# Kernel optimization log

Hardware: AMD Instinct MI355X
Metric: run time of the kernel (lower is better)

Reference implementation:

```python
import jax, jax.numpy as jnp
import numpy as np

N, D, K, E = 100000, 256, 16, 3200000
COLLAPSE_REG = 0.1


def setup_inputs() -> dict:
    key = jax.random.key(0)
    k1, k2, k3 = jax.random.split(key, 3)
    features = jax.random.normal(k1, (N, D), dtype=jnp.float32)
    edge_index = jax.random.randint(k2, (2, E), 0, N, dtype=jnp.int32)
    adj_vals = jnp.ones((E,), dtype=jnp.float32)
    # orthogonal-ish init for linear weight, zero bias (as in nn.init.orthogonal_/zeros_)
    W = jax.random.normal(k3, (K, D), dtype=jnp.float32) / np.sqrt(D).astype(np.float32)
    b = jnp.zeros((K,), dtype=jnp.float32)
    return {"features": features, "edge_index": edge_index, "adj_vals": adj_vals, "W": W, "b": b}


def reference(features, edge_index, adj_vals, W, b):
    n = features.shape[0]
    k = W.shape[0]
    # cluster assignment: softmax(linear(features)); dropout_rate=0 -> identity
    assignments = jax.nn.softmax(features @ W.T + b, axis=-1)  # [n, k]

    rows, cols = edge_index[0], edge_index[1]
    # node degrees from sparse adjacency (row sums)
    degrees = jax.ops.segment_sum(adj_vals, rows, num_segments=n)  # [n]
    m2 = jnp.sum(degrees)  # 2m (total edge weight * 2)

    # SpMM: (A @ S) via edge-wise gather + segment-sum scatter
    AS = jax.ops.segment_sum(adj_vals[:, None] * assignments[cols], rows, num_segments=n)  # [n, k]
    graph_pooled = assignments.T @ AS  # [k, k] = S^T A S

    # modularity null-model normalizer: (S^T d)(d^T S) / 2m
    left = assignments.T @ degrees  # [k]
    normalizer = jnp.outer(left, left) / m2
    spectral_loss = -jnp.trace(graph_pooled - normalizer) / m2

    cluster_sizes = jnp.sum(assignments, axis=0)  # [k]
    collapse_loss = COLLAPSE_REG * (
        jnp.linalg.norm(cluster_sizes) / n * jnp.sqrt(jnp.float32(k)) - 1.0
    )

    # pooled cluster representations: selu((S / sizes)^T X)  -> [k, d]
    assignments_pooling = assignments / cluster_sizes  # broadcast over clusters
    features_pooled = jax.nn.selu(assignments_pooling.T @ features)
    return features_pooled, assignments, spectral_loss, collapse_loss
```

## Files before the change

### kernel.cpp

```cpp
#include <hip/hip_runtime.h>

#define N_NODES 100000
#define DIM 256
#define KC 16
#define NE 3200000
#define CHUNK 64
#define NCHUNKS ((N_NODES + CHUNK - 1) / CHUNK)

using bf16x8 = __attribute__((ext_vector_type(8))) short;
using f32x4  = __attribute__((ext_vector_type(4))) float;

__device__ __forceinline__ float bflo(unsigned u) { return __uint_as_float(u << 16); }
__device__ __forceinline__ unsigned short f2bf(float f) {
    unsigned u = __float_as_uint(f);
    return (unsigned short)((u + 0x7fffu + ((u >> 16) & 1u)) >> 16);
}
__device__ __forceinline__ unsigned packbf(float a, float b) {
    return (unsigned)f2bf(a) | ((unsigned)f2bf(b) << 16);
}

template <bool WRITE_PACK>
__global__ __launch_bounds__(256) void k_assign_stx(const float4* __restrict__ X4,
                                                    const float4* __restrict__ W4,
                                                    const float* __restrict__ bias,
                                                    float* __restrict__ S,
                                                    unsigned* __restrict__ Sb,
                                                    float* __restrict__ cs_g,
                                                    float* __restrict__ stx) {
    __shared__ unsigned short Xbf[CHUNK * 264];
    __shared__ float ps[CHUNK * 20];
    __shared__ float csred[4][KC];

    const int lane = threadIdx.x & 63;
    const int wv   = threadIdx.x >> 6;
    const int col  = lane & 15;
    const int quad = lane >> 4;
    const int d    = threadIdx.x;

    bf16x8 wfrag[8];
    #pragma unroll
    for (int s = 0; s < 8; s++) {
        float4 wa = W4[col * 64 + s * 8 + quad * 2];
        float4 wb = W4[col * 64 + s * 8 + quad * 2 + 1];
        union { bf16x8 v; unsigned u[4]; } wf;
        wf.u[0] = packbf(wa.x, wa.y);
        wf.u[1] = packbf(wa.z, wa.w);
        wf.u[2] = packbf(wb.x, wb.y);
        wf.u[3] = packbf(wb.z, wb.w);
        wfrag[s] = wf.v;
    }
    const float bk = bias[col];

    float st[KC];
    #pragma unroll
    for (int k = 0; k < KC; k++) st[k] = 0.f;
    float csacc = 0.f;

    for (int ch = blockIdx.x; ch < NCHUNKS; ch += gridDim.x) {
        const int base = ch * CHUNK;
        __syncthreads();

        {
            const int c4 = threadIdx.x & 63;
            const int r0 = threadIdx.x >> 6;
            #pragma unroll 4
            for (int s = 0; s < 16; s++) {
                int r = r0 + 4 * s;
                int rg = base + r;
                if (rg >= N_NODES) rg = N_NODES - 1;
                float4 x = X4[(size_t)rg * 64 + c4];
                *((uint2*)&Xbf[r * 264 + c4 * 4]) =
                    make_uint2(packbf(x.x, x.y), packbf(x.z, x.w));
            }
        }
        __syncthreads();

        f32x4 acc = {0.f, 0.f, 0.f, 0.f};
        #pragma unroll
        for (int s = 0; s < 8; s++) {
            bf16x8 a = *(const bf16x8*)&Xbf[(wv * 16 + col) * 264 + s * 32 + quad * 8];
            acc = __builtin_amdgcn_mfma_f32_16x16x32_bf16(a, wfrag[s], acc, 0, 0, 0);
        }
        #pragma unroll
        for (int r = 0; r < 4; r++) {
            float lg = acc[r] + bk;
            float m = lg;
            #pragma unroll
            for (int off = 8; off >= 1; off >>= 1) m = fmaxf(m, __shfl_xor(m, off));
            float e = __expf(lg - m);
            float ssum = e;
            #pragma unroll
            for (int off = 8; off >= 1; off >>= 1) ssum += __shfl_xor(ssum, off);
            float pv = e / ssum;

            int nd = base + wv * 16 + quad * 4 + r;
            bool val = (nd < N_NODES);
            if (!val) pv = 0.f;
            if (val) S[(size_t)nd * KC + col] = pv;
            ps[(wv * 16 + quad * 4 + r) * 20 + col] = pv;
            csacc += pv;
            if (WRITE_PACK) {
                unsigned qb = __float2uint_rn(pv * 255.f);
                unsigned p01 = qb | (((unsigned)__shfl_xor((int)qb, 1)) << 8);
                unsigned p0123 = p01 | (((unsigned)__shfl_xor((int)p01, 2)) << 16);
                if (val && !(col & 3))
                    Sb[(size_t)nd * 4 + (col >> 2)] = p0123;
            }
        }
        __syncthreads();

        #pragma unroll 4
        for (int i = 0; i < CHUNK; i++) {
            float x = bflo((unsigned)Xbf[i * 264 + d]);
            const float4* pp = (const float4*)&ps[i * 20];
            float4 p0 = pp[0], p1 = pp[1], p2 = pp[2], p3 = pp[3];
            st[0]  += p0.x * x; st[1]  += p0.y * x; st[2]  += p0.z * x; st[3]  += p0.w * x;
            st[4]  += p1.x * x; st[5]  += p1.y * x; st[6]  += p1.z * x; st[7]  += p1.w * x;
            st[8]  += p2.x * x; st[9]  += p2.y * x; st[10] += p2.z * x; st[11] += p2.w * x;
            st[12] += p3.x * x; st[13] += p3.y * x; st[14] += p3.z * x; st[15] += p3.w * x;
        }
    }

    #pragma unroll
    for (int k = 0; k < KC; k++) atomicAdd(&stx[k * DIM + d], st[k]);

    csacc += __shfl_xor(csacc, 16);
    csacc += __shfl_xor(csacc, 32);
    if (lane < KC) csred[wv][col] = csacc;
    __syncthreads();
    if (threadIdx.x < KC) {
        int t = threadIdx.x;
        atomicAdd(&cs_g[t], csred[0][t] + csred[1][t] + csred[2][t] + csred[3][t]);
    }
}

__device__ __forceinline__ void edge_acc_u8(uint4 qr, uint4 qc, float a,
                                            float (&lf)[KC], float& m2l, float& trl) {
    union { uint4 v; unsigned w[4]; } R, C;
    R.v = qr; C.v = qc;
    float dd = 0.f;
    #pragma unroll
    for (int q = 0; q < 4; q++) {
        unsigned x = R.w[q], y = C.w[q];
        float s0 = (float)(x & 0xffu);
        float s1 = (float)((x >> 8) & 0xffu);
        float s2 = (float)((x >> 16) & 0xffu);
        float s3 = (float)(x >> 24);
        float c0 = (float)(y & 0xffu);
        float c1 = (float)((y >> 8) & 0xffu);
        float c2 = (float)((y >> 16) & 0xffu);
        float c3 = (float)(y >> 24);
        dd = fmaf(s0, c0, dd); dd = fmaf(s1, c1, dd);
        dd = fmaf(s2, c2, dd); dd = fmaf(s3, c3, dd);
        lf[4 * q + 0] = fmaf(a, s0, lf[4 * q + 0]);
        lf[4 * q + 1] = fmaf(a, s1, lf[4 * q + 1]);
        lf[4 * q + 2] = fmaf(a, s2, lf[4 * q + 2]);
        lf[4 * q + 3] = fmaf(a, s3, lf[4 * q + 3]);
    }
    m2l += a;
    trl = fmaf(a, dd, trl);
}

__global__ __launch_bounds__(256) void k_edges_u8(const int* __restrict__ rows,
                                                  const int* __restrict__ cols,
                                                  const float* __restrict__ adj,
                                                  const uint4* __restrict__ Sb4,
                                                  float* __restrict__ m2_g,
                                                  float* __restrict__ tr_g,
                                                  float* __restrict__ left_g) {
    float m2l = 0.f, trl = 0.f;
    float lf[KC];
    #pragma unroll
    for (int k = 0; k < KC; k++) lf[k] = 0.f;

    const int NU = NE / 2;
    const int stride = gridDim.x * blockDim.x;
    for (int u = blockIdx.x * blockDim.x + threadIdx.x; u < NU; u += stride) {
        int2   r2 = *(const int2*)(rows + 2 * (size_t)u);
        int2   c2 = *(const int2*)(cols + 2 * (size_t)u);
        float2 a2 = *(const float2*)(adj + 2 * (size_t)u);
        uint4 qr0 = Sb4[r2.x];
        uint4 qc0 = Sb4[c2.x];
        uint4 qr1 = Sb4[r2.y];
        uint4 qc1 = Sb4[c2.y];
        edge_acc_u8(qr0, qc0, a2.x, lf, m2l, trl);
        edge_acc_u8(qr1, qc1, a2.y, lf, m2l, trl);
    }

    trl *= (1.f / 65025.f);
    #pragma unroll
    for (int k = 0; k < KC; k++) lf[k] *= (1.f / 255.f);

    #pragma unroll
    for (int off = 32; off >= 1; off >>= 1) {
        m2l += __shfl_xor(m2l, off);
        trl += __shfl_xor(trl, off);
    }
    #pragma unroll
    for (int k = 0; k < KC; k++) {
        float v = lf[k];
        #pragma unroll
        for (int off = 32; off >= 1; off >>= 1) v += __shfl_xor(v, off);
        lf[k] = v;
    }
    __shared__ float red[4][18];
    int w = threadIdx.x >> 6;
    if ((threadIdx.x & 63) == 0) {
        red[w][0] = m2l; red[w][1] = trl;
        #pragma unroll
        for (int k = 0; k < KC; k++) red[w][2 + k] = lf[k];
    }
    __syncthreads();
    int t = threadIdx.x;
    if (t < 18) {
        float v = red[0][t] + red[1][t] + red[2][t] + red[3][t];
        float* dst = (t == 0) ? m2_g : (t == 1) ? tr_g : &left_g[t - 2];
        atomicAdd(dst, v);
    }
}

__global__ __launch_bounds__(256) void k_edges_f32(const int* __restrict__ rows,
                                                   const int* __restrict__ cols,
                                                   const float* __restrict__ adj,
                                                   const float* __restrict__ S,
                                                   float* __restrict__ m2_g,
                                                   float* __restrict__ tr_g,
                                                   float* __restrict__ left_g) {
    float m2l = 0.f, trl = 0.f;
    float lf[KC];
    #pragma unroll
    for (int k = 0; k < KC; k++) lf[k] = 0.f;

    int stride = gridDim.x * blockDim.x;
    for (int e = blockIdx.x * blockDim.x + threadIdx.x; e < NE; e += stride) {
        int r = rows[e], c = cols[e];
        float a = adj[e];
        float sv[KC], cv[KC];
        const float4* sr = (const float4*)(S + (size_t)r * KC);
        const float4* sc = (const float4*)(S + (size_t)c * KC);
        #pragma unroll
        for (int qq = 0; qq < 4; qq++) {
            float4 s4 = sr[qq], c4 = sc[qq];
            sv[4*qq]=s4.x; sv[4*qq+1]=s4.y; sv[4*qq+2]=s4.z; sv[4*qq+3]=s4.w;
            cv[4*qq]=c4.x; cv[4*qq+1]=c4.y; cv[4*qq+2]=c4.z; cv[4*qq+3]=c4.w;
        }
        float dd = 0.f;
        #pragma unroll
        for (int k = 0; k < KC; k++) {
            dd += sv[k] * cv[k];
            lf[k] += a * sv[k];
        }
        m2l += a;
        trl += a * dd;
    }

    #pragma unroll
    for (int off = 32; off >= 1; off >>= 1) {
        m2l += __shfl_xor(m2l, off);
        trl += __shfl_xor(trl, off);
    }
    #pragma unroll
    for (int k = 0; k < KC; k++) {
        float v = lf[k];
        #pragma unroll
        for (int off = 32; off >= 1; off >>= 1) v += __shfl_xor(v, off);
        lf[k] = v;
    }
    __shared__ float red[4][18];
    int w = threadIdx.x >> 6;
    if ((threadIdx.x & 63) == 0) {
        red[w][0] = m2l; red[w][1] = trl;
        #pragma unroll
        for (int k = 0; k < KC; k++) red[w][2 + k] = lf[k];
    }
    __syncthreads();
    int t = threadIdx.x;
    if (t < 18) {
        float v = red[0][t] + red[1][t] + red[2][t] + red[3][t];
        float* dst = (t == 0) ? m2_g : (t == 1) ? tr_g : &left_g[t - 2];
        atomicAdd(dst, v);
    }
}

__global__ __launch_bounds__(256) void k_final(const float* __restrict__ cs,
                                               const float* __restrict__ left,
                                               const float* __restrict__ m2p,
                                               const float* __restrict__ trp,
                                               const float* __restrict__ stx,
                                               float* __restrict__ out) {
    int t = threadIdx.x;
    #pragma unroll
    for (int k = 0; k < KC; k++) {
        float v = stx[k * DIM + t] / cs[k];
        float r = (v > 0.f) ? 1.0507009873554805f * v
                            : 1.7580993408473766f * (__expf(v) - 1.f);
        out[k * DIM + t] = r;
    }
    if (t == 0) {
        float m2 = *m2p;
        float tn = 0.f;
        #pragma unroll
        for (int k = 0; k < KC; k++) tn += left[k] * left[k];
        tn /= m2;
        float spectral = -((*trp) - tn) / m2;
        float ss = 0.f;
        #pragma unroll
        for (int k = 0; k < KC; k++) ss += cs[k] * cs[k];
        float collapse = 0.1f * (sqrtf(ss) / (float)N_NODES * 4.0f - 1.0f);
        out[KC * DIM + (size_t)N_NODES * KC]     = spectral;
        out[KC * DIM + (size_t)N_NODES * KC + 1] = collapse;
    }
}

extern "C" void kernel_launch(void* const* d_in, const int* in_sizes, int n_in,
                              void* d_out, int out_size, void* d_ws, size_t ws_size,
                              hipStream_t stream) {
    (void)out_size;

    const float* X    = nullptr;
    const int*   ei   = nullptr;
    const float* adj  = nullptr;
    const float* W    = nullptr;
    const float* bias = nullptr;
    for (int i = 0; i < n_in; i++) {
        switch (in_sizes[i]) {
            case 25600000: X    = (const float*)d_in[i]; break;
            case  6400000: ei   = (const int*)d_in[i];   break;
            case  3200000: adj  = (const float*)d_in[i]; break;
            case     4096: W    = (const float*)d_in[i]; break;
            case       16: bias = (const float*)d_in[i]; break;
        }
    }

    float* out = (float*)d_out;
    float* S   = out + KC * DIM;
    const int* rows = ei;
    const int* cols = ei + NE;

    float* ws   = (float*)d_ws;
    float* cs   = ws;
    float* left = ws + 16;
    float* m2   = ws + 32;
    float* tr   = ws + 33;
    float* stx  = ws + 64;
    unsigned* Sb = (unsigned*)(ws + 64 + KC * DIM);
    const size_t need = (64 + KC * DIM) * sizeof(float) + (size_t)N_NODES * 16;
    const bool use_pack = (ws_size >= need);

    hipMemsetAsync(d_ws, 0, (64 + KC * DIM) * sizeof(float), stream);

    const int agrid = 782;
    if (use_pack) {
        k_assign_stx<true><<<agrid, 256, 0, stream>>>(
            (const float4*)X, (const float4*)W, bias, S, Sb, cs, stx);
        k_edges_u8<<<2048, 256, 0, stream>>>(rows, cols, adj, (const uint4*)Sb,
                                             m2, tr, left);
    } else {
        k_assign_stx<false><<<agrid, 256, 0, stream>>>(
            (const float4*)X, (const float4*)W, bias, S, Sb, cs, stx);
        k_edges_f32<<<2048, 256, 0, stream>>>(rows, cols, adj, S, m2, tr, left);
    }
    k_final<<<1, 256, 0, stream>>>(cs, left, m2, tr, stx, out);
}
```

Baseline: 253.0 us.

## Compute S^T X with bf16 split-precision MFMA and transpose logits MFMA layout

Replaces the scalar FMA loop that accumulates S^T X per feature column with MFMA instructions. The assignment probabilities are split into hi and lo bf16 parts so the product keeps near-fp32 precision. The logits MFMA is transposed so each lane holds four clusters of one node, which lets the softmax use fewer shuffles and lets S and the packed Sb be written with vector stores. X is staged in shared memory in a new blocked layout to serve both MFMA operand patterns. The cost is scattered 16-bit LDS gathers to build the B fragments, plus more MFMA issue.

```diff
diff --git a/kernel.cpp b/kernel.cpp
--- a/kernel.cpp
+++ b/kernel.cpp
@@ -7,10 +7,14 @@
 #define CHUNK 64
 #define NCHUNKS ((N_NODES + CHUNK - 1) / CHUNK)
 
+#define D0STR 1168
+#define GSTR  144
+#define PSTR  72
+#define PLANE (16 * PSTR)
+
 using bf16x8 = __attribute__((ext_vector_type(8))) short;
 using f32x4  = __attribute__((ext_vector_type(4))) float;
 
-__device__ __forceinline__ float bflo(unsigned u) { return __uint_as_float(u << 16); }
 __device__ __forceinline__ unsigned short f2bf(float f) {
     unsigned u = __float_as_uint(f);
     return (unsigned short)((u + 0x7fffu + ((u >> 16) & 1u)) >> 16);
@@ -27,21 +31,20 @@
                                                     unsigned* __restrict__ Sb,
                                                     float* __restrict__ cs_g,
                                                     float* __restrict__ stx) {
-    __shared__ unsigned short Xbf[CHUNK * 264];
-    __shared__ float ps[CHUNK * 20];
+    __shared__ __align__(16) unsigned short Xs[16 * D0STR];
+    __shared__ __align__(16) unsigned short psb[2 * 16 * PSTR];
     __shared__ float csred[4][KC];
 
     const int lane = threadIdx.x & 63;
     const int wv   = threadIdx.x >> 6;
-    const int col  = lane & 15;
+    const int c    = lane & 15;
     const int quad = lane >> 4;
-    const int d    = threadIdx.x;
 
     bf16x8 wfrag[8];
     #pragma unroll
     for (int s = 0; s < 8; s++) {
-        float4 wa = W4[col * 64 + s * 8 + quad * 2];
-        float4 wb = W4[col * 64 + s * 8 + quad * 2 + 1];
+        float4 wa = W4[c * 64 + s * 8 + quad * 2];
+        float4 wb = W4[c * 64 + s * 8 + quad * 2 + 1];
         union { bf16x8 v; unsigned u[4]; } wf;
         wf.u[0] = packbf(wa.x, wa.y);
         wf.u[1] = packbf(wa.z, wa.w);
@@ -49,84 +52,126 @@
         wf.u[3] = packbf(wb.z, wb.w);
         wfrag[s] = wf.v;
     }
-    const float bk = bias[col];
-
-    float st[KC];
-    #pragma unroll
-    for (int k = 0; k < KC; k++) st[k] = 0.f;
-    float csacc = 0.f;
+    const float4 b4 = ((const float4*)bias)[quad];
+
+    f32x4 acc[4];
+    #pragma unroll
+    for (int t = 0; t < 4; t++) acc[t] = (f32x4){0.f, 0.f, 0.f, 0.f};
+    float csr[4] = {0.f, 0.f, 0.f, 0.f};
 
     for (int ch = blockIdx.x; ch < NCHUNKS; ch += gridDim.x) {
         const int base = ch * CHUNK;
         __syncthreads();
 
         {
-            const int c4 = threadIdx.x & 63;
-            const int r0 = threadIdx.x >> 6;
+            const int c4  = threadIdx.x & 63;
+            const int r0  = threadIdx.x >> 6;
+            const int d0s = c4 >> 2;
+            const int wo  = (c4 & 3) * 4;
             #pragma unroll 4
             for (int s = 0; s < 16; s++) {
                 int r = r0 + 4 * s;
                 int rg = base + r;
                 if (rg >= N_NODES) rg = N_NODES - 1;
                 float4 x = X4[(size_t)rg * 64 + c4];
-                *((uint2*)&Xbf[r * 264 + c4 * 4]) =
+                *(uint2*)&Xs[d0s * D0STR + (r >> 3) * GSTR + (r & 7) * 16 + wo] =
                     make_uint2(packbf(x.x, x.y), packbf(x.z, x.w));
             }
         }
         __syncthreads();
 
-        f32x4 acc = {0.f, 0.f, 0.f, 0.f};
-        #pragma unroll
-        for (int s = 0; s < 8; s++) {
-            bf16x8 a = *(const bf16x8*)&Xbf[(wv * 16 + col) * 264 + s * 32 + quad * 8];
-            acc = __builtin_amdgcn_mfma_f32_16x16x32_bf16(a, wfrag[s], acc, 0, 0, 0);
+        f32x4 la = {0.f, 0.f, 0.f, 0.f};
+        {
+            const int node = wv * 16 + c;
+            const int gA = node >> 3, n8 = node & 7;
+            #pragma unroll
+            for (int s = 0; s < 8; s++) {
+                const int d0 = 2 * s + (quad >> 1);
+                bf16x8 xf = *(const bf16x8*)&Xs[d0 * D0STR + gA * GSTR + n8 * 16 + (quad & 1) * 8];
+                la = __builtin_amdgcn_mfma_f32_16x16x32_bf16(wfrag[s], xf, la, 0, 0, 0);
+            }
+        }
+        float lg0 = la[0] + b4.x, lg1 = la[1] + b4.y;
+        float lg2 = la[2] + b4.z, lg3 = la[3] + b4.w;
+        float mx = fmaxf(fmaxf(lg0, lg1), fmaxf(lg2, lg3));
+        mx = fmaxf(mx, __shfl_xor(mx, 16));
+        mx = fmaxf(mx, __shfl_xor(mx, 32));
+        float e0 = __expf(lg0 - mx), e1 = __expf(lg1 - mx);
+        float e2 = __expf(lg2 - mx), e3 = __expf(lg3 - mx);
+        float ssum = e0 + e1 + e2 + e3;
+        ssum += __shfl_xor(ssum, 16);
+        ssum += __shfl_xor(ssum, 32);
+        float inv = 1.f / ssum;
+        float pvv[4] = {e0 * inv, e1 * inv, e2 * inv, e3 * inv};
+
+        const int nn = wv * 16 + c;
+        const int nd = base + nn;
+        if (nd >= N_NODES) {
+            pvv[0] = pvv[1] = pvv[2] = pvv[3] = 0.f;
+        } else {
+            *(float4*)&S[(size_t)nd * KC + quad * 4] =
+                make_float4(pvv[0], pvv[1], pvv[2], pvv[3]);
+            if (WRITE_PACK) {
+                unsigned q0 = __float2uint_rn(pvv[0] * 255.f);
+                unsigned q1 = __float2uint_rn(pvv[1] * 255.f);
+                unsigned q2 = __float2uint_rn(pvv[2] * 255.f);
+                unsigned q3 = __float2uint_rn(pvv[3] * 255.f);
+                Sb[(size_t)nd * 4 + quad] = q0 | (q1 << 8) | (q2 << 16) | (q3 << 24);
+            }
         }
         #pragma unroll
         for (int r = 0; r < 4; r++) {
-            float lg = acc[r] + bk;
-            float m = lg;
+            unsigned short ph = f2bf(pvv[r]);
+            float pl = pvv[r] - __uint_as_float(((unsigned)ph) << 16);
+            psb[(quad * 4 + r) * PSTR + nn] = ph;
+            psb[PLANE + (quad * 4 + r) * PSTR + nn] = f2bf(pl);
+            csr[r] += pvv[r];
+        }
+        __syncthreads();
+
+        bf16x8 afH[2], afL[2];
+        #pragma unroll
+        for (int ks = 0; ks < 2; ks++) {
+            afH[ks] = *(const bf16x8*)&psb[c * PSTR + ks * 32 + quad * 8];
+            afL[ks] = *(const bf16x8*)&psb[PLANE + c * PSTR + ks * 32 + quad * 8];
+        }
+        #pragma unroll
+        for (int t = 0; t < 4; t++) {
+            const int d0  = wv * 4 + t;
+            const int dlo = c;
+            union { bf16x8 v; unsigned short h[8]; } bf0, bf1;
             #pragma unroll
-            for (int off = 8; off >= 1; off >>= 1) m = fmaxf(m, __shfl_xor(m, off));
-            float e = __expf(lg - m);
-            float ssum = e;
-            #pragma unroll
-            for (int off = 8; off >= 1; off >>= 1) ssum += __shfl_xor(ssum, off);
-            float pv = e / ssum;
-
-            int nd = base + wv * 16 + quad * 4 + r;
-            bool val = (nd < N_NODES);
-            if (!val) pv = 0.f;
-            if (val) S[(size_t)nd * KC + col] = pv;
-            ps[(wv * 16 + quad * 4 + r) * 20 + col] = pv;
-            csacc += pv;
-            if (WRITE_PACK) {
-                unsigned qb = __float2uint_rn(pv * 255.f);
-                unsigned p01 = qb | (((unsigned)__shfl_xor((int)qb, 1)) << 8);
-                unsigned p0123 = p01 | (((unsigned)__shfl_xor((int)p01, 2)) << 16);
-                if (val && !(col & 3))
-                    Sb[(size_t)nd * 4 + (col >> 2)] = p0123;
+            for (int j = 0; j < 8; j++) {
+                const int n0 = quad * 8 + j;
+                bf0.h[j] = Xs[d0 * D0STR + (n0 >> 3) * GSTR + (n0 & 7) * 16 + dlo];
+                const int n1 = 32 + n0;
+                bf1.h[j] = Xs[d0 * D0STR + (n1 >> 3) * GSTR + (n1 & 7) * 16 + dlo];
             }
-        }
-        __syncthreads();
-
-        #pragma unroll 4
-        for (int i = 0; i < CHUNK; i++) {
-            float x = bflo((unsigned)Xbf[i * 264 + d]);
-            const float4* pp = (const float4*)&ps[i * 20];
-            float4 p0 = pp[0], p1 = pp[1], p2 = pp[2], p3 = pp[3];
-            st[0]  += p0.x * x; st[1]  += p0.y * x; st[2]  += p0.z * x; st[3]  += p0.w * x;
-            st[4]  += p1.x * x; st[5]  += p1.y * x; st[6]  += p1.z * x; st[7]  += p1.w * x;
-            st[8]  += p2.x * x; st[9]  += p2.y * x; st[10] += p2.z * x; st[11] += p2.w * x;
-            st[12] += p3.x * x; st[13] += p3.y * x; st[14] += p3.z * x; st[15] += p3.w * x;
-        }
-    }
-
-    #pragma unroll
-    for (int k = 0; k < KC; k++) atomicAdd(&stx[k * DIM + d], st[k]);
-
-    csacc += __shfl_xor(csacc, 16);
-    csacc += __shfl_xor(csacc, 32);
-    if (lane < KC) csred[wv][col] = csacc;
+            acc[t] = __builtin_amdgcn_mfma_f32_16x16x32_bf16(afH[0], bf0.v, acc[t], 0, 0, 0);
+            acc[t] = __builtin_amdgcn_mfma_f32_16x16x32_bf16(afL[0], bf0.v, acc[t], 0, 0, 0);
+            acc[t] = __builtin_amdgcn_mfma_f32_16x16x32_bf16(afH[1], bf1.v, acc[t], 0, 0, 0);
+            acc[t] = __builtin_amdgcn_mfma_f32_16x16x32_bf16(afL[1], bf1.v, acc[t], 0, 0, 0);
+        }
+    }
+
+    #pragma unroll
+    for (int t = 0; t < 4; t++) {
+        #pragma unroll
+        for (int r = 0; r < 4; r++)
+            atomicAdd(&stx[(quad * 4 + r) * DIM + (wv * 4 + t) * 16 + c], acc[t][r]);
+    }
+
+    #pragma unroll
+    for (int r = 0; r < 4; r++) {
+        float v = csr[r];
+        v += __shfl_xor(v, 1); v += __shfl_xor(v, 2);
+        v += __shfl_xor(v, 4); v += __shfl_xor(v, 8);
+        csr[r] = v;
+    }
+    if (c == 0) {
+        #pragma unroll
+        for (int r = 0; r < 4; r++) csred[wv][quad * 4 + r] = csr[r];
+    }
     __syncthreads();
     if (threadIdx.x < KC) {
         int t = threadIdx.x;
```

Result: no change. 248.7 us (-1.7%).
